# Performance work log

Measured on AMD Instinct MI355X. Metric: run time of the kernel, lower is better.

Reference implementation:

```python
import jax, jax.numpy as jnp
import numpy as np

D_MODEL = 1024
N_HEAD = 16
D_HEAD = D_MODEL // N_HEAD


def setup_inputs() -> dict:
    key = jax.random.key(0)
    k_x, k_qkv, k_proj = jax.random.split(key, 3)
    B, T = 2, 2048
    x = jax.random.normal(k_x, (B, T, D_MODEL), dtype=jnp.float32)
    # torch Linear weight [out, in]; y = x @ W.T. Scale ~ kaiming-uniform-ish.
    s = 1.0 / np.sqrt(D_MODEL)
    W_qkv = jax.random.uniform(k_qkv, (3 * D_MODEL, D_MODEL), dtype=jnp.float32, minval=-s, maxval=s)
    W_proj = jax.random.uniform(k_proj, (D_MODEL, D_MODEL), dtype=jnp.float32, minval=-s, maxval=s)
    return {"x": x, "W_qkv": W_qkv, "W_proj": W_proj}


def reference(x, W_qkv, W_proj):
    B, T, C = x.shape
    qkv = jnp.einsum('btc,oc->bto', x, W_qkv)  # [B,T,3C]
    q, k, v = jnp.split(qkv, 3, axis=-1)
    # [B,T,C] -> [B,H,T,Dh]
    def heads(t):
        return t.reshape(B, T, N_HEAD, D_HEAD).transpose(0, 2, 1, 3)
    q, k, v = heads(q), heads(k), heads(v)
    scale = 1.0 / np.sqrt(D_HEAD)
    scores = jnp.einsum('bhqd,bhkd->bhqk', q, k) * scale  # [B,H,T,T]
    causal = jnp.tril(jnp.ones((T, T), dtype=bool))
    scores = jnp.where(causal, scores, jnp.finfo(scores.dtype).min)
    attn = jax.nn.softmax(scores, axis=-1)
    y = jnp.einsum('bhqk,bhkd->bhqd', attn, v)  # [B,H,T,Dh]
    y = y.transpose(0, 2, 1, 3).reshape(B, T, C)
    return jnp.einsum('btc,oc->bto', y, W_proj)
```

## Files before the change

### kernel.cpp

```cpp
#include <hip/hip_runtime.h>

typedef unsigned short u16;
typedef float f32x4 __attribute__((ext_vector_type(4)));
typedef __bf16 bf16x8 __attribute__((ext_vector_type(8)));
typedef unsigned int u32x4 __attribute__((ext_vector_type(4)));
typedef u16 u16x4 __attribute__((ext_vector_type(4)));
typedef u16 u16x8 __attribute__((ext_vector_type(8)));

static __device__ __forceinline__ u16 f2bf(float f) {
  union { __bf16 h; u16 u; } c;
  c.h = (__bf16)f;
  return c.u;
}

static __device__ __forceinline__ void gload_lds16(const void* g, void* l) {
  __builtin_amdgcn_global_load_lds(
      (const __attribute__((address_space(1))) unsigned int*)g,
      (__attribute__((address_space(3))) unsigned int*)l, 16, 0, 0);
}

__global__ __launch_bounds__(256) void cvt3_f32_bf16(const float* __restrict__ a,
                                                     const float* __restrict__ bb,
                                                     const float* __restrict__ cc,
                                                     u16* __restrict__ out,
                                                     int n1, int n2, int n3) {
  int i = blockIdx.x * 256 + threadIdx.x;
  const float* src;
  int j = i;
  if (i < n1) { src = a; }
  else if (i < n1 + n2) { src = bb; j = i - n1; }
  else { src = cc; j = i - n1 - n2; if (j >= n3) return; }
  f32x4 v = *((const f32x4*)src + j);
  u16x4 o;
  o[0] = f2bf(v[0]); o[1] = f2bf(v[1]); o[2] = f2bf(v[2]); o[3] = f2bf(v[3]);
  *((u16x4*)out + i) = o;
}

template<int OUT_BF16, int FUSE_VT>
__global__ __launch_bounds__(256) void gemm_nt(const u16* __restrict__ A,
                                               const u16* __restrict__ B,
                                               void* __restrict__ Cp,
                                               u16* __restrict__ vt,
                                               int M, int N, int K, int gy) {
  __shared__ __align__(16) u16 lA[128 * 64];
  __shared__ __align__(16) u16 lB[128 * 64];
  const int tid = threadIdx.x;
  const int lane = tid & 63;
  const int wave = tid >> 6;
  const int wm = wave >> 1, wn = wave & 1;
  const int l15 = lane & 15, lg = lane >> 4;

  const int bid = blockIdx.x;
  const int xcd = bid & 7, s = bid >> 3;
  const int pnx = (N >> 7) >> 3;
  const int bm = (s % gy) * 128;
  const int bn = (xcd * pnx + s / gy) * 128;

  f32x4 acc[4][4];
#pragma unroll
  for (int i = 0; i < 4; ++i)
#pragma unroll
    for (int j = 0; j < 4; ++j) acc[i][j] = (f32x4){0.f, 0.f, 0.f, 0.f};

  const u16* Ag[4];
  const u16* Bg[4];
#pragma unroll
  for (int it = 0; it < 4; ++it) {
    const int ss = it * 256 + tid;
    const int row = ss >> 3, g = ss & 7;
    const int gsw = g ^ (row & 7);
    Ag[it] = A + (size_t)(bm + row) * K + gsw * 8;
    Bg[it] = B + (size_t)(bn + row) * K + gsw * 8;
  }

  for (int k0 = 0; k0 < K; k0 += 64) {
#pragma unroll
    for (int it = 0; it < 4; ++it) {
      gload_lds16(Ag[it] + k0, (u16*)lA + (size_t)(it * 256 + tid) * 8);
      gload_lds16(Bg[it] + k0, (u16*)lB + (size_t)(it * 256 + tid) * 8);
    }
    __syncthreads();
#pragma unroll
    for (int kk = 0; kk < 2; ++kk) {
      bf16x8 af[4], bfv[4];
#pragma unroll
      for (int mf = 0; mf < 4; ++mf) {
        const int row = wm * 64 + mf * 16 + l15;
        af[mf] = *(const bf16x8*)((const char*)lA + row * 128 +
                                  ((kk * 64 + lg * 16) ^ ((row & 7) << 4)));
      }
#pragma unroll
      for (int nf = 0; nf < 4; ++nf) {
        const int row = wn * 64 + nf * 16 + l15;
        bfv[nf] = *(const bf16x8*)((const char*)lB + row * 128 +
                                   ((kk * 64 + lg * 16) ^ ((row & 7) << 4)));
      }
#pragma unroll
      for (int mf = 0; mf < 4; ++mf)
#pragma unroll
        for (int nf = 0; nf < 4; ++nf)
          acc[mf][nf] = __builtin_amdgcn_mfma_f32_16x16x32_bf16(af[mf], bfv[nf], acc[mf][nf], 0, 0, 0);
    }
    __syncthreads();
  }

  if (FUSE_VT && bn >= 2048) {
#pragma unroll
    for (int mf = 0; mf < 4; ++mf) {
      const int row0 = bm + wm * 64 + mf * 16 + lg * 4;
      const int b = row0 >> 11, t0 = row0 & 2047;
#pragma unroll
      for (int nf = 0; nf < 4; ++nf) {
        const int colv = bn - 2048 + wn * 64 + nf * 16 + l15;
        const int h = colv >> 6, d = colv & 63;
        u16x4 pk;
        pk[0] = f2bf(acc[mf][nf][0]); pk[1] = f2bf(acc[mf][nf][1]);
        pk[2] = f2bf(acc[mf][nf][2]); pk[3] = f2bf(acc[mf][nf][3]);
        *(u16x4*)&vt[((size_t)((b * 16 + h) * 64 + d)) * 2048 + t0] = pk;
      }
    }
  } else {
#pragma unroll
    for (int mf = 0; mf < 4; ++mf) {
#pragma unroll
      for (int r = 0; r < 4; ++r) {
        const int row = bm + wm * 64 + mf * 16 + lg * 4 + r;
#pragma unroll
        for (int nf = 0; nf < 4; ++nf) {
          const int col = bn + wn * 64 + nf * 16 + l15;
          const float v = acc[mf][nf][r];
          if (OUT_BF16) ((u16*)Cp)[(size_t)row * N + col] = f2bf(v);
          else          ((float*)Cp)[(size_t)row * N + col] = v;
        }
      }
    }
  }
}

__global__ __launch_bounds__(512) void attn_fwd(const u16* __restrict__ qkv,
                                                const u16* __restrict__ vt,
                                                u16* __restrict__ y) {
  constexpr int T = 2048, C = 1024, C3 = 3072, D = 64;
  __shared__ __align__(16) u16 lK[2][64 * 64];
  __shared__ __align__(16) u16 lV[2][64 * 64];
  __shared__ __align__(16) u16 lP[8 * 16 * 64];
  const int tid = threadIdx.x, lane = tid & 63, w = tid >> 6;
  const int l15 = lane & 15, lg = lane >> 4;

  const int bid = blockIdx.x;
  const int xcd = bid & 7, slot = bid >> 3;
  const int bh = xcd * 4 + (slot >> 3);
  const int pi = slot & 7;
  const int b = bh >> 4, h = bh & 15;

  const int r0 = tid >> 3, off0 = (tid & 7) * 8;
  const int sb0 = (off0 * 2) ^ ((r0 & 7) << 4);
  const u16* Kbase = qkv + (size_t)b * T * C3 + C + h * D;
  const u16* Vbase = vt + (size_t)bh * D * T;
  char* lPb = (char*)lP + w * 2048;

  const float qscale = 0.125f * 1.44269504088896f;

#pragma unroll 1
  for (int qi = 0; qi < 2; ++qi) {
    const int qt = (qi == 0) ? pi : (15 - pi);
    const int q0 = qt * 128;
    const int nkt = 2 * qt + 2;
    const int qrow = q0 + w * 16 + l15;

    const size_t qoff = ((size_t)b * T + qrow) * C3 + h * D;
    const bf16x8 aq0 = *(const bf16x8*)&qkv[qoff + lg * 8];
    const bf16x8 aq1 = *(const bf16x8*)&qkv[qoff + 32 + lg * 8];

    float m = -1.0e30f, l = 0.f;
    f32x4 o_acc[4];
#pragma unroll
    for (int nf = 0; nf < 4; ++nf) o_acc[nf] = (f32x4){0.f, 0.f, 0.f, 0.f};

    u32x4 rk0 = *(const u32x4*)(Kbase + (size_t)r0 * C3 + off0);
    u32x4 rv0 = *(const u32x4*)(Vbase + (size_t)r0 * T + off0);
    __syncthreads();
    *(u32x4*)&lK[0][(r0 * 128 + sb0) >> 1] = rk0;
    *(u32x4*)&lV[0][(r0 * 128 + sb0) >> 1] = rv0;
    if (nkt > 1) {
      rk0 = *(const u32x4*)(Kbase + (size_t)(64 + r0) * C3 + off0);
      rv0 = *(const u32x4*)(Vbase + (size_t)r0 * T + 64 + off0);
    }

    for (int kt = 0; kt < nkt; ++kt) {
      const int cur = kt & 1;
      __syncthreads();
      if (kt < nkt - 1) {
        *(u32x4*)&lK[cur ^ 1][(r0 * 128 + sb0) >> 1] = rk0;
        *(u32x4*)&lV[cur ^ 1][(r0 * 128 + sb0) >> 1] = rv0;
        if (kt + 1 < nkt - 1) {
          const int kn = (kt + 2) * 64;
          rk0 = *(const u32x4*)(Kbase + (size_t)(kn + r0) * C3 + off0);
          rv0 = *(const u32x4*)(Vbase + (size_t)r0 * T + kn + off0);
        }
      }
      const u16* Kc = lK[cur];
      const u16* Vc = lV[cur];

      f32x4 s[4];
#pragma unroll
      for (int nf = 0; nf < 4; ++nf) s[nf] = (f32x4){0.f, 0.f, 0.f, 0.f};
      __builtin_amdgcn_s_setprio(1);
#pragma unroll
      for (int nf = 0; nf < 4; ++nf) {
        const int row = nf * 16 + l15;
        const int x = (row & 7) << 4;
        bf16x8 bk0 = *(const bf16x8*)&Kc[(row * 128 + ((lg * 16) ^ x)) >> 1];
        bf16x8 bk1 = *(const bf16x8*)&Kc[(row * 128 + ((64 + lg * 16) ^ x)) >> 1];
        s[nf] = __builtin_amdgcn_mfma_f32_16x16x32_bf16(bk0, aq0, s[nf], 0, 0, 0);
        s[nf] = __builtin_amdgcn_mfma_f32_16x16x32_bf16(bk1, aq1, s[nf], 0, 0, 0);
      }
      __builtin_amdgcn_s_setprio(0);

      if (kt >= 2 * qt) {
        const int kb = kt * 64;
#pragma unroll
        for (int nf = 0; nf < 4; ++nf)
#pragma unroll
          for (int r = 0; r < 4; ++r) {
            float v = s[nf][r] * qscale;
            if (kb + nf * 16 + lg * 4 + r > qrow) v = -1.0e30f;
            s[nf][r] = v;
          }
      } else {
#pragma unroll
        for (int nf = 0; nf < 4; ++nf)
#pragma unroll
          for (int r = 0; r < 4; ++r) s[nf][r] *= qscale;
      }

      float t0a = fmaxf(fmaxf(s[0][0], s[0][1]), fmaxf(s[0][2], s[0][3]));
      float t1a = fmaxf(fmaxf(s[1][0], s[1][1]), fmaxf(s[1][2], s[1][3]));
      float t2a = fmaxf(fmaxf(s[2][0], s[2][1]), fmaxf(s[2][2], s[2][3]));
      float t3a = fmaxf(fmaxf(s[3][0], s[3][1]), fmaxf(s[3][2], s[3][3]));
      float pmax = fmaxf(fmaxf(t0a, t1a), fmaxf(t2a, t3a));
      pmax = fmaxf(pmax, __shfl_xor(pmax, 16));
      pmax = fmaxf(pmax, __shfl_xor(pmax, 32));

      if (!__all(pmax <= m)) {
        const float mnew = fmaxf(m, pmax);
        const float fct = __builtin_amdgcn_exp2f(m - mnew);
        m = mnew;
        l *= fct;
#pragma unroll
        for (int r = 0; r < 4; ++r) {
          const float fr = __shfl(fct, lg * 4 + r);
#pragma unroll
          for (int nf = 0; nf < 4; ++nf) o_acc[nf][r] *= fr;
        }
      }

      float p[4][4];
#pragma unroll
      for (int nf = 0; nf < 4; ++nf)
#pragma unroll
        for (int r = 0; r < 4; ++r) p[nf][r] = __builtin_amdgcn_exp2f(s[nf][r] - m);
      float s0a = (p[0][0] + p[0][1]) + (p[0][2] + p[0][3]);
      float s1a = (p[1][0] + p[1][1]) + (p[1][2] + p[1][3]);
      float s2a = (p[2][0] + p[2][1]) + (p[2][2] + p[2][3]);
      float s3a = (p[3][0] + p[3][1]) + (p[3][2] + p[3][3]);
      float psum = (s0a + s1a) + (s2a + s3a);
      psum += __shfl_xor(psum, 16);
      psum += __shfl_xor(psum, 32);
      l += psum;

#pragma unroll
      for (int nf = 0; nf < 4; ++nf) {
        u16x4 pk;
        pk[0] = f2bf(p[nf][0]); pk[1] = f2bf(p[nf][1]);
        pk[2] = f2bf(p[nf][2]); pk[3] = f2bf(p[nf][3]);
        *(u16x4*)(lPb + l15 * 128 + ((nf * 32 + lg * 8) ^ ((l15 & 7) << 4))) = pk;
      }

      __builtin_amdgcn_s_setprio(1);
#pragma unroll
      for (int sj = 0; sj < 2; ++sj) {
        bf16x8 ap = *(const bf16x8*)(lPb + l15 * 128 + ((sj * 64 + lg * 16) ^ ((l15 & 7) << 4)));
#pragma unroll
        for (int nf = 0; nf < 4; ++nf) {
          const int d = nf * 16 + l15;
          bf16x8 bv = *(const bf16x8*)&Vc[(d * 128 + ((sj * 64 + lg * 16) ^ ((d & 7) << 4))) >> 1];
          o_acc[nf] = __builtin_amdgcn_mfma_f32_16x16x32_bf16(ap, bv, o_acc[nf], 0, 0, 0);
        }
      }
      __builtin_amdgcn_s_setprio(0);
    }

#pragma unroll
    for (int r = 0; r < 4; ++r) {
      const float li = __builtin_amdgcn_rcpf(__shfl(l, lg * 4 + r));
      const int row = q0 + w * 16 + lg * 4 + r;
#pragma unroll
      for (int nf = 0; nf < 4; ++nf) {
        const int col = h * D + nf * 16 + l15;
        y[((size_t)b * T + row) * C + col] = f2bf(o_acc[nf][r] * li);
      }
    }
  }
}

extern "C" void kernel_launch(void* const* d_in, const int* in_sizes, int n_in,
                              void* d_out, int out_size, void* d_ws, size_t ws_size,
                              hipStream_t stream) {
  const float* x = (const float*)d_in[0];
  const float* Wqkv = (const float*)d_in[1];
  const float* Wproj = (const float*)d_in[2];
  float* out = (float*)d_out;

  constexpr int B = 2, T = 2048, C = 1024, C3 = 3072, H = 16, D = 64;
  constexpr int M = B * T;

  u16* xb = (u16*)d_ws;
  u16* wqkvb = xb + (size_t)M * C;
  u16* wprojb = wqkvb + (size_t)C3 * C;
  u16* qkvb = wprojb + (size_t)C * C;
  u16* vtb = qkvb + (size_t)M * C3;
  u16* yb = vtb + (size_t)M * C;

  constexpr int n1 = (M * C) / 4, n2 = (C3 * C) / 4, n3 = (C * C) / 4;
  cvt3_f32_bf16<<<dim3((n1 + n2 + n3 + 255) / 256), 256, 0, stream>>>(
      x, Wqkv, Wproj, xb, n1, n2, n3);

  gemm_nt<1, 1><<<dim3((C3 / 128) * (M / 128)), 256, 0, stream>>>(
      xb, wqkvb, qkvb, vtb, M, C3, C, M / 128);
  attn_fwd<<<dim3(256), 512, 0, stream>>>(qkvb, vtb, yb);
  gemm_nt<0, 0><<<dim3((C / 128) * (M / 128)), 256, 0, stream>>>(
      yb, wprojb, out, nullptr, M, C, C, M / 128);
}
```

Before: 112.8 us.

## Split attention KV range in two halves and merge partial outputs

Splits each query tile's causal KV loop into two halves handled by separate blocks, doubling the attention grid to 512 blocks. Each half writes a normalized partial output in bf16 plus its running max and sum. A new merge kernel combines the halves with log-sum-exp weights. The aim is more parallelism and occupancy across CUs. The cost is an extra kernel launch, the extra memory traffic for the partial outputs, and some precision loss from storing the partials in bf16.

```diff
diff --git a/kernel.cpp b/kernel.cpp
--- a/kernel.cpp
+++ b/kernel.cpp
@@ -11,6 +11,11 @@
   union { __bf16 h; u16 u; } c;
   c.h = (__bf16)f;
   return c.u;
+}
+static __device__ __forceinline__ float bf2f(u16 u) {
+  union { unsigned u; float f; } c;
+  c.u = ((unsigned)u) << 16;
+  return c.f;
 }
 
 static __device__ __forceinline__ void gload_lds16(const void* g, void* l) {
@@ -139,7 +144,8 @@
 
 __global__ __launch_bounds__(512) void attn_fwd(const u16* __restrict__ qkv,
                                                 const u16* __restrict__ vt,
-                                                u16* __restrict__ y) {
+                                                u16* __restrict__ po,
+                                                float* __restrict__ mlf) {
   constexpr int T = 2048, C = 1024, C3 = 3072, D = 64;
   __shared__ __align__(16) u16 lK[2][64 * 64];
   __shared__ __align__(16) u16 lV[2][64 * 64];
@@ -149,8 +155,9 @@
 
   const int bid = blockIdx.x;
   const int xcd = bid & 7, slot = bid >> 3;
-  const int bh = xcd * 4 + (slot >> 3);
-  const int pi = slot & 7;
+  const int bh = xcd * 4 + (slot >> 4);
+  const int rem = slot & 15;
+  const int pi = rem >> 1, hf = rem & 1;
   const int b = bh >> 4, h = bh & 15;
 
   const int r0 = tid >> 3, off0 = (tid & 7) * 8;
@@ -165,7 +172,9 @@
   for (int qi = 0; qi < 2; ++qi) {
     const int qt = (qi == 0) ? pi : (15 - pi);
     const int q0 = qt * 128;
-    const int nkt = 2 * qt + 2;
+    const int kts = hf ? (qt + 1) : 0;
+    const int kte = hf ? (2 * qt + 2) : (qt + 1);
+    const int nit = kte - kts;
     const int qrow = q0 + w * 16 + l15;
 
     const size_t qoff = ((size_t)b * T + qrow) * C3 + h * D;
@@ -177,23 +186,24 @@
 #pragma unroll
     for (int nf = 0; nf < 4; ++nf) o_acc[nf] = (f32x4){0.f, 0.f, 0.f, 0.f};
 
-    u32x4 rk0 = *(const u32x4*)(Kbase + (size_t)r0 * C3 + off0);
-    u32x4 rv0 = *(const u32x4*)(Vbase + (size_t)r0 * T + off0);
+    u32x4 rk0 = *(const u32x4*)(Kbase + (size_t)(kts * 64 + r0) * C3 + off0);
+    u32x4 rv0 = *(const u32x4*)(Vbase + (size_t)r0 * T + kts * 64 + off0);
     __syncthreads();
     *(u32x4*)&lK[0][(r0 * 128 + sb0) >> 1] = rk0;
     *(u32x4*)&lV[0][(r0 * 128 + sb0) >> 1] = rv0;
-    if (nkt > 1) {
-      rk0 = *(const u32x4*)(Kbase + (size_t)(64 + r0) * C3 + off0);
-      rv0 = *(const u32x4*)(Vbase + (size_t)r0 * T + 64 + off0);
-    }
-
-    for (int kt = 0; kt < nkt; ++kt) {
-      const int cur = kt & 1;
+    if (nit > 1) {
+      rk0 = *(const u32x4*)(Kbase + (size_t)((kts + 1) * 64 + r0) * C3 + off0);
+      rv0 = *(const u32x4*)(Vbase + (size_t)r0 * T + (kts + 1) * 64 + off0);
+    }
+
+    for (int i = 0; i < nit; ++i) {
+      const int kt = kts + i;
+      const int cur = i & 1;
       __syncthreads();
-      if (kt < nkt - 1) {
+      if (i < nit - 1) {
         *(u32x4*)&lK[cur ^ 1][(r0 * 128 + sb0) >> 1] = rk0;
         *(u32x4*)&lV[cur ^ 1][(r0 * 128 + sb0) >> 1] = rv0;
-        if (kt + 1 < nkt - 1) {
+        if (i + 1 < nit - 1) {
           const int kn = (kt + 2) * 64;
           rk0 = *(const u32x4*)(Kbase + (size_t)(kn + r0) * C3 + off0);
           rv0 = *(const u32x4*)(Vbase + (size_t)r0 * T + kn + off0);
@@ -291,17 +301,47 @@
       __builtin_amdgcn_s_setprio(0);
     }
 
+    u16* pob = po + (size_t)hf * (4096ull * 1024ull);
 #pragma unroll
     for (int r = 0; r < 4; ++r) {
-      const float li = __builtin_amdgcn_rcpf(__shfl(l, lg * 4 + r));
+      const float lv = __shfl(l, lg * 4 + r);
+      const float li = (lv > 0.f) ? __builtin_amdgcn_rcpf(lv) : 0.f;
       const int row = q0 + w * 16 + lg * 4 + r;
 #pragma unroll
       for (int nf = 0; nf < 4; ++nf) {
         const int col = h * D + nf * 16 + l15;
-        y[((size_t)b * T + row) * C + col] = f2bf(o_acc[nf][r] * li);
-      }
+        pob[((size_t)b * T + row) * C + col] = f2bf(o_acc[nf][r] * li);
+      }
+    }
+    if (lg == 0) {
+      const size_t idx = (size_t)(b * T + qrow) * 16 + h;
+      float* mp = mlf + (size_t)hf * 131072ull + idx * 2;
+      mp[0] = m;
+      mp[1] = l;
     }
   }
+}
+
+__global__ __launch_bounds__(256) void merge_o(const u16* __restrict__ po,
+                                               const float* __restrict__ mlf,
+                                               u16* __restrict__ y) {
+  const int gid = blockIdx.x * 256 + threadIdx.x;
+  const int row = gid >> 3, d0 = (gid & 7) * 8;
+  const int bt = row >> 4, h = row & 15;
+  const float m1 = mlf[row * 2], l1 = mlf[row * 2 + 1];
+  const float m2 = mlf[131072 + row * 2], l2 = mlf[131072 + row * 2 + 1];
+  const float ms = fmaxf(m1, m2);
+  const float a1 = l1 * __builtin_amdgcn_exp2f(m1 - ms);
+  const float a2 = l2 * __builtin_amdgcn_exp2f(m2 - ms);
+  const float inv = __builtin_amdgcn_rcpf(a1 + a2);
+  const float w1 = a1 * inv, w2 = a2 * inv;
+  const size_t off = (size_t)bt * 1024 + h * 64 + d0;
+  u16x8 p1 = *(const u16x8*)&po[off];
+  u16x8 p2 = *(const u16x8*)&po[4194304ull + off];
+  u16x8 o;
+#pragma unroll
+  for (int j = 0; j < 8; ++j) o[j] = f2bf(w1 * bf2f(p1[j]) + w2 * bf2f(p2[j]));
+  *(u16x8*)&y[off] = o;
 }
 
 extern "C" void kernel_launch(void* const* d_in, const int* in_sizes, int n_in,
@@ -321,6 +361,8 @@
   u16* qkvb = wprojb + (size_t)C * C;
   u16* vtb = qkvb + (size_t)M * C3;
   u16* yb = vtb + (size_t)M * C;
+  u16* po = yb + (size_t)M * C;
+  float* mlf = (float*)(po + 2ull * M * C);
 
   constexpr int n1 = (M * C) / 4, n2 = (C3 * C) / 4, n3 = (C * C) / 4;
   cvt3_f32_bf16<<<dim3((n1 + n2 + n3 + 255) / 256), 256, 0, stream>>>(
@@ -328,7 +370,8 @@
 
   gemm_nt<1, 1><<<dim3((C3 / 128) * (M / 128)), 256, 0, stream>>>(
       xb, wqkvb, qkvb, vtb, M, C3, C, M / 128);
-  attn_fwd<<<dim3(256), 512, 0, stream>>>(qkvb, vtb, yb);
+  attn_fwd<<<dim3(512), 512, 0, stream>>>(qkvb, vtb, po, mlf);
+  merge_o<<<dim3(2048), 256, 0, stream>>>(po, mlf, yb);
   gemm_nt<0, 0><<<dim3((C / 128) * (M / 128)), 256, 0, stream>>>(
       yb, wprojb, out, nullptr, M, C, C, M / 128);
 }
```

Result: no change. 110.8 us (-1.8%).
